# Optimization experiments

Measured on AMD Instinct MI355X. Metric: run time of the kernel, lower is better.

The kernel has to match this reference:

```python
import jax, jax.numpy as jnp
import numpy as np

T, B, TD, HD, VD = 64, 4096, 512, 256, 484
LN_EPS = 1e-5   # torch nn.LayerNorm default
COS_EPS = 1e-8  # torch F.cosine_similarity default


def setup_inputs() -> dict:
    key = jax.random.key(0)
    ks = jax.random.split(key, 6)
    w = lambda k, shape: jax.random.normal(k, shape, dtype=jnp.float32) * 0.02
    return {
        "t_feat": jax.random.normal(ks[0], (B, TD), dtype=jnp.float32),
        "W1": w(ks[1], (T, HD, TD)),            # torch Linear weight layout [out, in]
        "b1": w(ks[2], (T, HD)),
        "gamma": jnp.ones((T, HD), jnp.float32),
        "beta": jnp.zeros((T, HD), jnp.float32),
        "W2": w(ks[3], (T, VD, HD)),
        "b2": w(ks[4], (T, VD)),
        "centroids": jax.random.normal(ks[5], (T, VD), dtype=jnp.float32),
    }


def reference(t_feat, W1, b1, gamma, beta, W2, b2, centroids):
    # All T per-task mappers batched into one grouped GEMM pipeline.
    # Linear1: [B, TD] x [T, HD, TD] -> [T, B, HD]
    h = jnp.einsum("bd,thd->tbh", t_feat, W1) + b1[:, None, :]
    # LayerNorm over hidden dim (per task affine params)
    mu = jnp.mean(h, axis=-1, keepdims=True)
    var = jnp.mean(jnp.square(h - mu), axis=-1, keepdims=True)
    h = (h - mu) * jax.lax.rsqrt(var + LN_EPS) * gamma[:, None, :] + beta[:, None, :]
    # Exact GELU (torch nn.GELU default uses erf)
    h = jax.nn.gelu(h, approximate=False)
    # Linear2: [T, B, HD] x [T, VD, HD] -> [T, B, VD] predicted visual features
    v = jnp.einsum("tbh,tvh->tbv", h, W2) + b2[:, None, :]
    # Cosine similarity vs each task centroid (eps-clamped norms, as in torch)
    v_norm = jnp.maximum(jnp.linalg.norm(v, axis=-1), COS_EPS)          # [T, B]
    c_norm = jnp.maximum(jnp.linalg.norm(centroids, axis=-1), COS_EPS)  # [T]
    cos = jnp.einsum("tbv,tv->tb", v, centroids) / (v_norm * c_norm[:, None])
    distances = jnp.mean(1.0 - cos, axis=-1)  # [T] mean cosine distance per task
    best_task = jnp.argmin(distances)          # top-1 routing decision
    return distances, best_task
```

## Files before the change

kernel.cpp:

```cpp
#include <hip/hip_runtime.h>
#include <math.h>

#define TASKS 64
#define NB    4096
#define TDI   512
#define HDI   256
#define VDI   484

#define WS_TF   ((size_t)0)
#define WS_W1   ((size_t)4194304)
#define WS_W2   ((size_t)20971520)
#define WS_CN   ((size_t)37748736)
#define WS_BC   ((size_t)37748992)
#define WS_ACC  ((size_t)37749248)

#define LDS_HP 0
#define LDS_B2 32768
#define LDS_R0 34816
#define LDS_R1 35840
#define LDS_MU 36864
#define LDS_RS 37120
#define SMEM_BYTES 37376

typedef _Float16 half8 __attribute__((ext_vector_type(8)));
typedef float    f32x4 __attribute__((ext_vector_type(4)));

#define MFMA16(a, b, c) __builtin_amdgcn_mfma_f32_16x16x32_f16((a), (b), (c), 0, 0, 0)

__device__ __forceinline__ half8 cvt8(float4 v0, float4 v1) {
  half8 r;
  r[0]=(_Float16)v0.x; r[1]=(_Float16)v0.y; r[2]=(_Float16)v0.z; r[3]=(_Float16)v0.w;
  r[4]=(_Float16)v1.x; r[5]=(_Float16)v1.y; r[6]=(_Float16)v1.z; r[7]=(_Float16)v1.w;
  return r;
}

__device__ __forceinline__ float gelu_exact(float x) {
  float az = fabsf(x) * 0.70710678118654752f;
  float d  = fmaf(0.3275911f, az, 1.0f);
  float t; asm("v_rcp_f32 %0, %1" : "=v"(t) : "v"(d));
  float p  = fmaf(t, 1.061405429f, -1.453152027f);
  p = fmaf(t, p, 1.421413741f);
  p = fmaf(t, p, -0.284496736f);
  p = fmaf(t, p, 0.254829592f);
  p = p * t;
  float m = az * az * -1.4426950408889634f;
  float e; asm("v_exp_f32 %0, %1" : "=v"(e) : "v"(m));
  float er = fmaf(-p, e, 1.0f);
  er = copysignf(er, x);
  float hx = 0.5f * x;
  return fmaf(hx, er, hx);
}

extern "C" __global__ void prep_all(const float* __restrict__ t_feat,
                                    const float* __restrict__ W1,
                                    const float* __restrict__ W2,
                                    const float* __restrict__ b2,
                                    const float* __restrict__ cent,
                                    _Float16* __restrict__ tf,
                                    _Float16* __restrict__ w1,
                                    _Float16* __restrict__ w2,
                                    float* __restrict__ cnorm,
                                    float* __restrict__ bc,
                                    float* __restrict__ accum) {
  const int bid = blockIdx.x, tid = threadIdx.x;
  __shared__ float redc[256], redb[256];
  if (bid < 1024) {
    int u = bid * 256 + tid;
    int row = u >> 6, k8 = u & 63;
    float4 v0 = ((const float4*)t_feat)[u * 2];
    float4 v1 = ((const float4*)t_feat)[u * 2 + 1];
    int rb = row >> 6, rt = (row >> 4) & 3, l15 = row & 15, ks = k8 >> 2, q = k8 & 3;
    size_t o = (size_t)rb * 4096 + ks * 256 + rt * 64 + q * 16 + l15;
    *(half8*)(tf + o * 8) = cvt8(v0, v1);
  } else if (bid < 5120) {
    int u = (bid - 1024) * 256 + tid;
    int t = u >> 14, rem = u & 16383, hd = rem >> 6, k8 = rem & 63;
    float4 v0 = ((const float4*)W1)[u * 2];
    float4 v1 = ((const float4*)W1)[u * 2 + 1];
    int w_ = hd >> 6, ct = (hd >> 4) & 3, l15 = hd & 15, ks = k8 >> 2, q = k8 & 3;
    size_t o = (size_t)t * 16384 + w_ * 4096 + ks * 256 + ct * 64 + q * 16 + l15;
    *(half8*)(w1 + o * 8) = cvt8(v0, v1);
  } else if (bid < 9216) {
    int u = (bid - 5120) * 256 + tid;
    int t = u >> 14, rem = u & 16383, vd = rem >> 5, k8 = rem & 31;
    half8 hv;
    if (vd < 484) {
      float4 v0 = ((const float4*)W2)[(size_t)(t * 484 + vd) * 64 + k8 * 2];
      float4 v1 = ((const float4*)W2)[(size_t)(t * 484 + vd) * 64 + k8 * 2 + 1];
      hv = cvt8(v0, v1);
    } else if (vd >= 485) {
      #pragma unroll
      for (int i = 0; i < 8; ++i) hv[i] = (_Float16)0.f;
    } else {
      return;
    }
    int pass = vd >> 8, w_ = (vd >> 6) & 3, ct = (vd >> 4) & 3, l15 = vd & 15;
    int ks = k8 >> 2, q = k8 & 3;
    size_t o = (size_t)t * 16384 + pass * 8192 + w_ * 2048 + ks * 256 + ct * 64 + q * 16 + l15;
    *(half8*)(w2 + o * 8) = hv;
  } else {
    int t = bid - 9216;
    int h = tid;
    float wcv = 0.f;
    for (int v = 0; v < VDI; ++v)
      wcv += W2[((size_t)t * VDI + v) * HDI + h] * cent[(size_t)t * VDI + v];
    {
      int ks = h >> 5, q = (h >> 3) & 3;
      size_t o = (size_t)t * 16384 + 8192 + 3 * 2048 + ks * 256 + 2 * 64 + q * 16 + 4;
      w2[o * 8 + (h & 7)] = (_Float16)wcv;
    }
    float c2 = 0.f, b2c = 0.f;
    for (int v = h; v < VDI; v += 256) {
      float c = cent[(size_t)t * VDI + v];
      c2 += c * c;
      b2c += b2[(size_t)t * VDI + v] * c;
    }
    redc[tid] = c2; redb[tid] = b2c;
    __syncthreads();
    if (tid < 64) {
      c2  = redc[tid] + redc[tid + 64] + redc[tid + 128] + redc[tid + 192];
      b2c = redb[tid] + redb[tid + 64] + redb[tid + 128] + redb[tid + 192];
      #pragma unroll
      for (int off = 32; off; off >>= 1) { c2 += __shfl_xor(c2, off); b2c += __shfl_xor(b2c, off); }
      if (tid == 0) { cnorm[t] = sqrtf(c2); bc[t] = b2c; accum[t] = 0.f; }
    }
  }
}


#define STEP_RELOAD(A, ACC, PB) do {                                           \
  _Pragma("unroll") for (int ct_ = 0; ct_ < 4; ++ct_) {                        \
    ACC[0][ct_] = MFMA16(A[0], b[ct_], ACC[0][ct_]);                           \
    ACC[1][ct_] = MFMA16(A[1], b[ct_], ACC[1][ct_]);                           \
    ACC[2][ct_] = MFMA16(A[2], b[ct_], ACC[2][ct_]);                           \
    ACC[3][ct_] = MFMA16(A[3], b[ct_], ACC[3][ct_]);                           \
    b[ct_] = (PB)[ct_ * 64];                                                   \
  } } while (0)

#define STEP_LAST(A, ACC) do {                                                 \
  _Pragma("unroll") for (int ct_ = 0; ct_ < 4; ++ct_) {                        \
    ACC[0][ct_] = MFMA16(A[0], b[ct_], ACC[0][ct_]);                           \
    ACC[1][ct_] = MFMA16(A[1], b[ct_], ACC[1][ct_]);                           \
    ACC[2][ct_] = MFMA16(A[2], b[ct_], ACC[2][ct_]);                           \
    ACC[3][ct_] = MFMA16(A[3], b[ct_], ACC[3][ct_]);                           \
  } } while (0)

#define LD_A4(D, P) do { D[0] = (P)[0]; D[1] = (P)[64]; D[2] = (P)[128]; D[3] = (P)[192]; } while (0)

extern "C" __global__ void __launch_bounds__(256, 4)
router_main(const half8* __restrict__ tfv,
            const half8* __restrict__ w1v,
            const half8* __restrict__ w2v,
            const float* __restrict__ b1,
            const float* __restrict__ gamma,
            const float* __restrict__ beta,
            const float* __restrict__ b2,
            const float* __restrict__ bc,
            const float* __restrict__ cnorm,
            float* __restrict__ accum) {
  __shared__ __align__(16) char smem[SMEM_BYTES];

  const int tid = threadIdx.x;
  const int bx  = blockIdx.x;
  const int t  = ((bx & 7) << 3) | (bx >> 9);
  const int rb = (bx >> 3) & 63;

  const int lane = tid & 63;
  const int w    = tid >> 6;
  const int quad = lane >> 4;
  const int l15  = lane & 15;

  {
    float* b2s = (float*)(smem + LDS_B2);
    int i0 = tid;
    b2s[i0] = (i0 < VDI) ? b2[(size_t)t * VDI + i0] : 0.f;
    int i1 = tid + 256;
    float v = 0.f;
    if (i1 < VDI) v = b2[(size_t)t * VDI + i1];
    else if (i1 == VDI) v = bc[t];
    b2s[i1] = v;
  }
  float b1v[4];
  #pragma unroll
  for (int ct = 0; ct < 4; ++ct)
    b1v[ct] = b1[t * HDI + w * 64 + ct * 16 + l15];

  f32x4 zero4 = {0.f, 0.f, 0.f, 0.f};
  f32x4 acc[4][4];
  #pragma unroll
  for (int rt = 0; rt < 4; ++rt)
    #pragma unroll
    for (int ct = 0; ct < 4; ++ct) acc[rt][ct] = zero4;

  half8 a0[4], a1[4], b[4];

  {
    const half8* pa = tfv + ((size_t)rb * 4096 + quad * 16 + l15);
    const half8* pb = w1v + ((size_t)t * 16384 + w * 4096 + quad * 16 + l15);
    LD_A4(a0, pa);
    b[0] = pb[0]; b[1] = pb[64]; b[2] = pb[128]; b[3] = pb[192];
    a1[0] = pa[256]; a1[1] = pa[320]; a1[2] = pa[384]; a1[3] = pa[448];
    pa += 512;
    pb += 256;
    #pragma unroll 1
    for (int ks = 0; ks < 14; ks += 2) {
      STEP_RELOAD(a0, acc, pb); pb += 256;
      LD_A4(a0, pa);            pa += 256;
      STEP_RELOAD(a1, acc, pb); pb += 256;
      LD_A4(a1, pa);            pa += 256;
    }
    STEP_RELOAD(a0, acc, pb);
    STEP_LAST(a1, acc);
  }

  float gv[4], bev[4];
  #pragma unroll
  for (int ct = 0; ct < 4; ++ct) {
    gv[ct]  = gamma[t * HDI + w * 64 + ct * 16 + l15];
    bev[ct] = beta [t * HDI + w * 64 + ct * 16 + l15];
  }
  {
    float* red0 = (float*)(smem + LDS_R0);
    float* red1 = (float*)(smem + LDS_R1);
    #pragma unroll
    for (int rt = 0; rt < 4; ++rt)
      #pragma unroll
      for (int r = 0; r < 4; ++r) {
        float sv = 0.f, qv = 0.f;
        #pragma unroll
        for (int ct = 0; ct < 4; ++ct) {
          float v = acc[rt][ct][r] + b1v[ct];
          acc[rt][ct][r] = v;
          sv += v; qv += v * v;
        }
        sv += __shfl_xor(sv, 1); qv += __shfl_xor(qv, 1);
        sv += __shfl_xor(sv, 2); qv += __shfl_xor(qv, 2);
        sv += __shfl_xor(sv, 4); qv += __shfl_xor(qv, 4);
        sv += __shfl_xor(sv, 8); qv += __shfl_xor(qv, 8);
        if (l15 == 0) {
          int m = rt * 16 + quad * 4 + r;
          red0[w * 64 + m] = sv;
          red1[w * 64 + m] = qv;
        }
      }
    __syncthreads();
    if (tid < 64) {
      float s = red0[tid] + red0[64 + tid] + red0[128 + tid] + red0[192 + tid];
      float q = red1[tid] + red1[64 + tid] + red1[128 + tid] + red1[192 + tid];
      float mu = s * (1.f / HDI);
      float var = q * (1.f / HDI) - mu * mu;
      ((float*)(smem + LDS_MU))[tid] = mu;
      ((float*)(smem + LDS_RS))[tid] = rsqrtf(var + 1e-5f);
    }
    __syncthreads();
    const float* mus = (const float*)(smem + LDS_MU);
    const float* rss = (const float*)(smem + LDS_RS);
    #pragma unroll
    for (int rt = 0; rt < 4; ++rt)
      #pragma unroll
      for (int ct = 0; ct < 4; ++ct) {
        int col = w * 64 + ct * 16 + l15;
        int base = (((col >> 5) * 4 + rt) * 4 + ((col >> 3) & 3)) * 256
                 + quad * 64 + (l15 & 7) * 2;
        #pragma unroll
        for (int r = 0; r < 4; ++r) {
          int m = rt * 16 + quad * 4 + r;
          float x = (acc[rt][ct][r] - mus[m]) * rss[m];
          x = x * gv[ct] + bev[ct];
          float g = gelu_exact(x);
          *(_Float16*)(smem + LDS_HP + base + r * 16) = (_Float16)g;
        }
      }
    __syncthreads();
  }

  {
    const float* b2s = (const float*)(smem + LDS_B2);
    float* red0 = (float*)(smem + LDS_R0);
    float* red1 = (float*)(smem + LDS_R1);
    const char* ha = smem + LDS_HP + quad * 256 + l15 * 16;

    #pragma unroll 1
    for (int pass = 0; pass < 2; ++pass) {
      const half8* pc = w2v + ((size_t)t * 16384 + pass * 8192 + w * 2048 + quad * 16 + l15);
      f32x4 acc2[4][4];
      #pragma unroll
      for (int rt = 0; rt < 4; ++rt)
        #pragma unroll
        for (int ct = 0; ct < 4; ++ct) acc2[rt][ct] = zero4;

      a0[0] = *(const half8*)(ha);        a0[1] = *(const half8*)(ha + 1024);
      a0[2] = *(const half8*)(ha + 2048); a0[3] = *(const half8*)(ha + 3072);
      b[0] = pc[0]; b[1] = pc[64]; b[2] = pc[128]; b[3] = pc[192];
      a1[0] = *(const half8*)(ha + 4096); a1[1] = *(const half8*)(ha + 5120);
      a1[2] = *(const half8*)(ha + 6144); a1[3] = *(const half8*)(ha + 7168);
      pc += 256;
      #pragma unroll 1
      for (int ks = 0; ks < 6; ks += 2) {
        STEP_RELOAD(a0, acc2, pc); pc += 256;
        {
          const char* h2 = ha + (ks + 2) * 4096;
          a0[0] = *(const half8*)(h2);        a0[1] = *(const half8*)(h2 + 1024);
          a0[2] = *(const half8*)(h2 + 2048); a0[3] = *(const half8*)(h2 + 3072);
        }
        STEP_RELOAD(a1, acc2, pc); pc += 256;
        {
          const char* h3 = ha + (ks + 3) * 4096;
          a1[0] = *(const half8*)(h3);        a1[1] = *(const half8*)(h3 + 1024);
          a1[2] = *(const half8*)(h3 + 2048); a1[3] = *(const half8*)(h3 + 3072);
        }
      }
      STEP_RELOAD(a0, acc2, pc);
      STEP_LAST(a1, acc2);

      #pragma unroll
      for (int rt = 0; rt < 4; ++rt)
        #pragma unroll
        for (int r = 0; r < 4; ++r) {
          float ssq = 0.f, dtv = 0.f;
          #pragma unroll
          for (int ct = 0; ct < 4; ++ct) {
            int vcol = pass * 256 + w * 64 + ct * 16 + l15;
            float val = acc2[rt][ct][r] + b2s[vcol];
            ssq += (vcol < VDI) ? val * val : 0.f;
            dtv += (vcol == VDI) ? val : 0.f;
          }
          ssq += __shfl_xor(ssq, 1); dtv += __shfl_xor(dtv, 1);
          ssq += __shfl_xor(ssq, 2); dtv += __shfl_xor(dtv, 2);
          ssq += __shfl_xor(ssq, 4); dtv += __shfl_xor(dtv, 4);
          ssq += __shfl_xor(ssq, 8); dtv += __shfl_xor(dtv, 8);
          if (l15 == 0) {
            int m = rt * 16 + quad * 4 + r;
            if (pass == 0) {
              red0[w * 64 + m] = ssq;
            } else {
              red0[w * 64 + m] += ssq;
              red1[w * 64 + m] = dtv;
            }
          }
        }
    }

    __syncthreads();
    if (tid < 64) {
      float ss  = red0[tid] + red0[64 + tid] + red0[128 + tid] + red0[192 + tid];
      float dot = red1[tid] + red1[64 + tid] + red1[128 + tid] + red1[192 + tid];
      float cn = fmaxf(cnorm[t], 1e-8f);
      float vn = fmaxf(sqrtf(ss), 1e-8f);
      float part = 1.0f - dot / (vn * cn);
      part += __shfl_down(part, 32);
      part += __shfl_down(part, 16);
      part += __shfl_down(part, 8);
      part += __shfl_down(part, 4);
      part += __shfl_down(part, 2);
      part += __shfl_down(part, 1);
      if (tid == 0) atomicAdd(accum + t, part);
    }
  }
}

extern "C" __global__ void finalize_k(const float* __restrict__ accum, float* __restrict__ out) {
  int t = threadIdx.x;
  float d = accum[t] * (1.0f / (float)NB);
  out[t] = d;
  float bd = d; int bi = t;
  #pragma unroll
  for (int off = 32; off; off >>= 1) {
    float od = __shfl_xor(bd, off);
    int   oi = __shfl_xor(bi, off);
    if (od < bd || (od == bd && oi < bi)) { bd = od; bi = oi; }
  }
  if (t == 0) out[64] = (float)bi;
}

extern "C" void kernel_launch(void* const* d_in, const int* in_sizes, int n_in,
                              void* d_out, int out_size, void* d_ws, size_t ws_size,
                              hipStream_t stream) {
  const float* t_feat = (const float*)d_in[0];
  const float* W1     = (const float*)d_in[1];
  const float* b1     = (const float*)d_in[2];
  const float* gamma  = (const float*)d_in[3];
  const float* beta   = (const float*)d_in[4];
  const float* W2     = (const float*)d_in[5];
  const float* b2     = (const float*)d_in[6];
  const float* cent   = (const float*)d_in[7];

  char* ws = (char*)d_ws;
  _Float16* tf = (_Float16*)(ws + WS_TF);
  _Float16* w1 = (_Float16*)(ws + WS_W1);
  _Float16* w2 = (_Float16*)(ws + WS_W2);
  float* cnorm = (float*)(ws + WS_CN);
  float* bc    = (float*)(ws + WS_BC);
  float* accum = (float*)(ws + WS_ACC);
  float* out = (float*)d_out;

  prep_all<<<9280, 256, 0, stream>>>(t_feat, W1, W2, b2, cent,
                                     tf, w1, w2, cnorm, bc, accum);
  router_main<<<4096, 256, 0, stream>>>((const half8*)tf, (const half8*)w1, (const half8*)w2,
                                        b1, gamma, beta, b2, bc, cnorm, accum);
  finalize_k<<<1, 64, 0, stream>>>(accum, out);
}
```

Baseline: 348.1 us.

## Coalesce prep stores, raise MFMA wave priority, defer bias loads past GEMM

The prep kernel now iterates over destination (swizzled) indices, so fp16 stores are fully coalesced while the fp32 source reads are gathered. The main kernel wraps its MFMA steps in s_setprio to favor math waves during the K-loop. The b1/b2 bias loads move after the first GEMM, which shortens the prologue and lowers register pressure during the loop. Gathered reads in prep may be less efficient than the old scattered writes, and the priority hints may have little effect.

```diff
diff --git a/kernel.cpp b/kernel.cpp
--- a/kernel.cpp
+++ b/kernel.cpp
@@ -65,28 +65,31 @@
   const int bid = blockIdx.x, tid = threadIdx.x;
   __shared__ float redc[256], redb[256];
   if (bid < 1024) {
-    int u = bid * 256 + tid;
-    int row = u >> 6, k8 = u & 63;
-    float4 v0 = ((const float4*)t_feat)[u * 2];
-    float4 v1 = ((const float4*)t_feat)[u * 2 + 1];
-    int rb = row >> 6, rt = (row >> 4) & 3, l15 = row & 15, ks = k8 >> 2, q = k8 & 3;
-    size_t o = (size_t)rb * 4096 + ks * 256 + rt * 64 + q * 16 + l15;
-    *(half8*)(tf + o * 8) = cvt8(v0, v1);
+    int p = bid * 256 + tid;
+    int rb = p >> 12, r = p & 4095;
+    int ks = r >> 8, rt = (r >> 6) & 3, q = (r >> 4) & 3, l15 = r & 15;
+    int row = rb * 64 + rt * 16 + l15, k8 = ks * 4 + q;
+    float4 v0 = ((const float4*)t_feat)[(row * 64 + k8) * 2];
+    float4 v1 = ((const float4*)t_feat)[(row * 64 + k8) * 2 + 1];
+    *(half8*)(tf + (size_t)p * 8) = cvt8(v0, v1);
   } else if (bid < 5120) {
-    int u = (bid - 1024) * 256 + tid;
-    int t = u >> 14, rem = u & 16383, hd = rem >> 6, k8 = rem & 63;
-    float4 v0 = ((const float4*)W1)[u * 2];
-    float4 v1 = ((const float4*)W1)[u * 2 + 1];
-    int w_ = hd >> 6, ct = (hd >> 4) & 3, l15 = hd & 15, ks = k8 >> 2, q = k8 & 3;
-    size_t o = (size_t)t * 16384 + w_ * 4096 + ks * 256 + ct * 64 + q * 16 + l15;
-    *(half8*)(w1 + o * 8) = cvt8(v0, v1);
+    int p = (bid - 1024) * 256 + tid;
+    int t = p >> 14, r = p & 16383;
+    int w_ = r >> 12, ks = (r >> 8) & 15, ct = (r >> 6) & 3, q = (r >> 4) & 3, l15 = r & 15;
+    int hd = w_ * 64 + ct * 16 + l15, k8 = ks * 4 + q;
+    float4 v0 = ((const float4*)W1)[((size_t)(t * 256 + hd) * 64 + k8) * 2];
+    float4 v1 = ((const float4*)W1)[((size_t)(t * 256 + hd) * 64 + k8) * 2 + 1];
+    *(half8*)(w1 + (size_t)p * 8) = cvt8(v0, v1);
   } else if (bid < 9216) {
-    int u = (bid - 5120) * 256 + tid;
-    int t = u >> 14, rem = u & 16383, vd = rem >> 5, k8 = rem & 31;
+    int p = (bid - 5120) * 256 + tid;
+    int t = p >> 14, r = p & 16383;
+    int pass = r >> 13, w_ = (r >> 11) & 3, ks = (r >> 8) & 7;
+    int ct = (r >> 6) & 3, q = (r >> 4) & 3, l15 = r & 15;
+    int vd = pass * 256 + w_ * 64 + ct * 16 + l15, k8 = ks * 4 + q;
     half8 hv;
     if (vd < 484) {
-      float4 v0 = ((const float4*)W2)[(size_t)(t * 484 + vd) * 64 + k8 * 2];
-      float4 v1 = ((const float4*)W2)[(size_t)(t * 484 + vd) * 64 + k8 * 2 + 1];
+      float4 v0 = ((const float4*)W2)[((size_t)(t * 484 + vd) * 64 + k8 * 2)];
+      float4 v1 = ((const float4*)W2)[((size_t)(t * 484 + vd) * 64 + k8 * 2) + 1];
       hv = cvt8(v0, v1);
     } else if (vd >= 485) {
       #pragma unroll
@@ -94,10 +97,7 @@
     } else {
       return;
     }
-    int pass = vd >> 8, w_ = (vd >> 6) & 3, ct = (vd >> 4) & 3, l15 = vd & 15;
-    int ks = k8 >> 2, q = k8 & 3;
-    size_t o = (size_t)t * 16384 + pass * 8192 + w_ * 2048 + ks * 256 + ct * 64 + q * 16 + l15;
-    *(half8*)(w2 + o * 8) = hv;
+    *(half8*)(w2 + (size_t)p * 8) = hv;
   } else {
     int t = bid - 9216;
     int h = tid;
@@ -129,21 +129,27 @@
 
 
 #define STEP_RELOAD(A, ACC, PB) do {                                           \
+  __builtin_amdgcn_s_setprio(1);                                               \
   _Pragma("unroll") for (int ct_ = 0; ct_ < 4; ++ct_) {                        \
     ACC[0][ct_] = MFMA16(A[0], b[ct_], ACC[0][ct_]);                           \
     ACC[1][ct_] = MFMA16(A[1], b[ct_], ACC[1][ct_]);                           \
     ACC[2][ct_] = MFMA16(A[2], b[ct_], ACC[2][ct_]);                           \
     ACC[3][ct_] = MFMA16(A[3], b[ct_], ACC[3][ct_]);                           \
     b[ct_] = (PB)[ct_ * 64];                                                   \
-  } } while (0)
+  }                                                                            \
+  __builtin_amdgcn_s_setprio(0);                                               \
+} while (0)
 
 #define STEP_LAST(A, ACC) do {                                                 \
+  __builtin_amdgcn_s_setprio(1);                                               \
   _Pragma("unroll") for (int ct_ = 0; ct_ < 4; ++ct_) {                        \
     ACC[0][ct_] = MFMA16(A[0], b[ct_], ACC[0][ct_]);                           \
     ACC[1][ct_] = MFMA16(A[1], b[ct_], ACC[1][ct_]);                           \
     ACC[2][ct_] = MFMA16(A[2], b[ct_], ACC[2][ct_]);                           \
     ACC[3][ct_] = MFMA16(A[3], b[ct_], ACC[3][ct_]);                           \
-  } } while (0)
+  }                                                                            \
+  __builtin_amdgcn_s_setprio(0);                                               \
+} while (0)
 
 #define LD_A4(D, P) do { D[0] = (P)[0]; D[1] = (P)[64]; D[2] = (P)[128]; D[3] = (P)[192]; } while (0)
 
@@ -169,21 +175,6 @@
   const int w    = tid >> 6;
   const int quad = lane >> 4;
   const int l15  = lane & 15;
-
-  {
-    float* b2s = (float*)(smem + LDS_B2);
-    int i0 = tid;
-    b2s[i0] = (i0 < VDI) ? b2[(size_t)t * VDI + i0] : 0.f;
-    int i1 = tid + 256;
-    float v = 0.f;
-    if (i1 < VDI) v = b2[(size_t)t * VDI + i1];
-    else if (i1 == VDI) v = bc[t];
-    b2s[i1] = v;
-  }
-  float b1v[4];
-  #pragma unroll
-  for (int ct = 0; ct < 4; ++ct)
-    b1v[ct] = b1[t * HDI + w * 64 + ct * 16 + l15];
 
   f32x4 zero4 = {0.f, 0.f, 0.f, 0.f};
   f32x4 acc[4][4];
@@ -213,11 +204,22 @@
     STEP_LAST(a1, acc);
   }
 
-  float gv[4], bev[4];
+  float b1v[4], gv[4], bev[4];
   #pragma unroll
   for (int ct = 0; ct < 4; ++ct) {
+    b1v[ct] = b1   [t * HDI + w * 64 + ct * 16 + l15];
     gv[ct]  = gamma[t * HDI + w * 64 + ct * 16 + l15];
     bev[ct] = beta [t * HDI + w * 64 + ct * 16 + l15];
+  }
+  {
+    float* b2s = (float*)(smem + LDS_B2);
+    int i0 = tid;
+    b2s[i0] = (i0 < VDI) ? b2[(size_t)t * VDI + i0] : 0.f;
+    int i1 = tid + 256;
+    float v = 0.f;
+    if (i1 < VDI) v = b2[(size_t)t * VDI + i1];
+    else if (i1 == VDI) v = bc[t];
+    b2s[i1] = v;
   }
   {
     float* red0 = (float*)(smem + LDS_R0);
```

Result: no change. 344.5 us (-1.0%).
